# Optimization experiments

Measured on AMD Instinct MI355X. Metric: run time of the kernel, lower is better.

## Reference

```python
import jax, jax.numpy as jnp
import numpy as np

EPS = 1e-5

def _bn(x, s, b, m, v):
    # inference-mode BatchNorm2d over channel axis of NCHW
    return (x - m[None, :, None, None]) * jax.lax.rsqrt(v[None, :, None, None] + EPS) \
           * s[None, :, None, None] + b[None, :, None, None]

def _conv3(x, w):
    return jax.lax.conv_general_dilated(x, w, (1, 1), 'SAME',
                                        dimension_numbers=('NCHW', 'OIHW', 'NCHW'))

def _conv1(x, w, b):
    # 1x1 conv as einsum; w: [out_c, in_c]
    return jnp.einsum('oc,bchw->bohw', w, x) + b[None, :, None, None]

def _cca(f, qw, qb, kw, kb, vw, vb, gamma):
    # Criss-cross attention (faithful to source: no diagonal -inf masking, INF() unused there)
    B, C, H, W = f.shape
    q = _conv1(f, qw, qb)   # [B, C/8, H, W]
    k = _conv1(f, kw, kb)   # [B, C/8, H, W]
    v = _conv1(f, vw, vb)   # [B, C,   H, W]
    # energy along column (same w, all h') and row (same h, all w')
    eH = jnp.einsum('bchw,bciw->bhwi', q, k)            # [B,H,W,H]
    eW = jnp.einsum('bchw,bchj->bhwj', q, k)            # [B,H,W,W]
    att = jax.nn.softmax(jnp.concatenate([eH, eW], axis=3), axis=3)  # [B,H,W,H+W]
    aH, aW = att[..., :H], att[..., H:]
    oH = jnp.einsum('bhwi,bciw->bchw', aH, v)
    oW = jnp.einsum('bhwj,bchj->bchw', aW, v)
    return gamma * (oH + oW) + f


def setup_inputs() -> dict:
    key = jax.random.key(0)
    ks = iter(jax.random.split(key, 64))
    B, Cin, H, W = 8, 2048, 64, 64
    Ci, Cq, Co = 256, 32, 512
    rn = lambda s, sc=0.02: jax.random.normal(next(ks), s, jnp.float32) * sc
    ru = lambda s: jax.random.uniform(next(ks), s, jnp.float32)
    return {
        'x': jax.random.normal(next(ks), (B, Cin, H, W), jnp.float32),
        'recurrence': 2,
        'conva_w': rn((Ci, Cin, 3, 3)),
        'bn_a_s': ru((Ci,)), 'bn_a_b': rn((Ci,), 0.1), 'bn_a_m': rn((Ci,), 0.1), 'bn_a_v': ru((Ci,)),
        'q_w': rn((Cq, Ci)), 'q_b': rn((Cq,), 0.1),
        'k_w': rn((Cq, Ci)), 'k_b': rn((Cq,), 0.1),
        'v_w': rn((Ci, Ci)), 'v_b': rn((Ci,), 0.1),
        'cca_gamma': rn((1,), 1.0),
        'convb_w': rn((Ci, Ci, 3, 3)),
        'bn_b_s': ru((Ci,)), 'bn_b_b': rn((Ci,), 0.1), 'bn_b_m': rn((Ci,), 0.1), 'bn_b_v': ru((Ci,)),
        'sq_w': rn((Ci, Ci)), 'sq_b': rn((Ci,), 0.1),
        'bn_g_s': ru((Ci,)), 'bn_g_b': rn((Ci,), 0.1), 'bn_g_m': rn((Ci,), 0.1), 'bn_g_v': ru((Ci,)),
        'fc1_w': rn((Ci // 2, Ci)), 'fc1_b': rn((Ci // 2,), 0.1),
        'fc2_w': rn((Ci, Ci // 2)), 'fc2_b': rn((Ci,), 0.1),
        'bott_w': rn((Co, Cin + 2 * Ci, 3, 3)),
        'bn_t_s': ru((Co,)), 'bn_t_b': rn((Co,), 0.1), 'bn_t_m': rn((Co,), 0.1), 'bn_t_v': ru((Co,)),
    }


def reference(x, recurrence, conva_w, bn_a_s, bn_a_b, bn_a_m, bn_a_v,
              q_w, q_b, k_w, k_b, v_w, v_b, cca_gamma,
              convb_w, bn_b_s, bn_b_b, bn_b_m, bn_b_v,
              sq_w, sq_b, bn_g_s, bn_g_b, bn_g_m, bn_g_v,
              fc1_w, fc1_b, fc2_w, fc2_b,
              bott_w, bn_t_s, bn_t_b, bn_t_m, bn_t_v):
    out = _bn(_conv3(x, conva_w), bn_a_s, bn_a_b, bn_a_m, bn_a_v)
    # Global_Avg_Pooling (SE gating) on conva output
    fm = jax.nn.relu(_bn(_conv1(out, sq_w, sq_b), bn_g_s, bn_g_b, bn_g_m, bn_g_v))
    vec = fm.mean(axis=(-2, -1))                       # [B, Ci]
    h = jax.nn.relu(vec @ fc1_w.T + fc1_b)
    gate = jax.nn.sigmoid(h @ fc2_w.T + fc2_b)
    out_gap = out * gate[:, :, None, None]
    # recurrent criss-cross attention
    for _ in range(recurrence):
        out = _cca(out, q_w, q_b, k_w, k_b, v_w, v_b, cca_gamma)
    out = _bn(_conv3(out, convb_w), bn_b_s, bn_b_b, bn_b_m, bn_b_v)
    cat = jnp.concatenate([x, out, out_gap], axis=1)   # [B, Cin+2*Ci, H, W]
    return _bn(_conv3(cat, bott_w), bn_t_s, bn_t_b, bn_t_m, bn_t_v)
```

## Files before the change

### kernel.cpp

```cpp
#include <hip/hip_runtime.h>
#include <hip/hip_bf16.h>

typedef unsigned short u16;
typedef unsigned int u32;
typedef __attribute__((ext_vector_type(8))) short short8;
typedef __attribute__((ext_vector_type(8))) unsigned short u16x8;
typedef __attribute__((ext_vector_type(4))) float f32x4;

#define BN_EPS 1e-5f
#define PADW 66
#define CATC 2560

__device__ __forceinline__ u16 f2b(float f) {
    __hip_bfloat16 h = __float2bfloat16(f);
    return *reinterpret_cast<u16*>(&h);
}
__device__ __forceinline__ float b2f(u16 u) {
    __hip_bfloat16 h;
    *reinterpret_cast<u16*>(&h) = u;
    return __bfloat162float(h);
}
__device__ __forceinline__ void async_copy16(void* lds, const void* g) {
    __builtin_amdgcn_global_load_lds((const __attribute__((address_space(1))) u32*)g,
                                     (__attribute__((address_space(3))) u32*)lds, 16, 0, 0);
}
__device__ __forceinline__ void fence_() { asm volatile("" ::: "memory"); }
__device__ __forceinline__ void barrier_() { fence_(); __builtin_amdgcn_s_barrier(); fence_(); }

template<int TAPS, int BN, int EPI, int CPT, int NN>
__global__ __launch_bounds__(512, 2)
void gemm8(const u16* __restrict__ Ag, int cstride,
           const u16* __restrict__ Bg, int ktot,
           const float* __restrict__ alpha, const float* __restrict__ beta,
           u16* __restrict__ outb, int ostride, int ochoff,
           float* __restrict__ outf, int nch)
{
    constexpr int WN   = BN / 4;
    constexpr int NSUB = WN / 16;
    constexpr int NQ   = NSUB / 2;
    constexpr int BLH  = BN / 128;
    constexpr int ASZ  = 256 * 128;
    constexpr int BSZ  = BN * 128;
    const int KT = ktot / 64;

    extern __shared__ __align__(16) char smem[];
    char* smA = smem;
    char* smB = smem + 2 * ASZ;

    const int tid  = threadIdx.x;
    const int lane = tid & 63;
    const int wave = tid >> 6;
    const int wr = wave >> 2;
    const int wc = wave & 3;

    const int nwg = gridDim.x;
    const int wg  = blockIdx.x;
    const int swz = (wg & 7) * (nwg >> 3) + (wg >> 3);
    const int m0 = (swz / NN) * 256;
    const int n0 = (swz % NN) * BN;

    const int sr = tid >> 3;
    const int sc = tid & 7;
    const int scx8 = (sc ^ (sr & 7)) * 8;
    long apix[4];
#pragma unroll
    for (int j = 0; j < 4; ++j) {
        int p = m0 + j * 64 + sr;
        int b = p >> 12, h = (p >> 6) & 63, w = p & 63;
        apix[j] = (TAPS == 1) ? ((long)(b * PADW + h + 1) * PADW + (w + 1))
                              : ((long)(b * PADW + h) * PADW + w);
    }
    long brow[2 * BLH];
#pragma unroll
    for (int h = 0; h < 2; ++h)
#pragma unroll
        for (int l = 0; l < BLH; ++l)
            brow[h * BLH + l] = (long)(n0 + h * (BN / 2) + l * 64 + sr) * ktot;

    auto stA = [&](int bsel, int h, int c0, long toff) {
#pragma unroll
        for (int l = 0; l < 2; ++l) {
            const u16* g = Ag + (apix[2 * h + l] + toff) * cstride + c0 + scx8;
            async_copy16(smA + bsel * ASZ + h * 16384 + l * 8192 + tid * 16, g);
        }
    };
    auto stB = [&](int bsel, int h, int k0) {
#pragma unroll
        for (int l = 0; l < BLH; ++l) {
            const u16* g = Bg + brow[h * BLH + l] + k0 + scx8;
            async_copy16(smB + bsel * BSZ + h * (BSZ / 2) + l * 8192 + tid * 16, g);
        }
    };

    const int rsel  = lane & 15;
    const int cswz0 = (((lane >> 4)     ^ (lane & 7)) << 4);
    const int cswz1 = (((4 | (lane >> 4)) ^ (lane & 7)) << 4);

    f32x4 acc[8][NSUB] = {};
    short8 a[4][2], b0[NQ][2], b1[NQ][2];

    auto ldA = [&](int bsel, int mh) {
        const char* base = smA + bsel * ASZ + (wr * 128 + mh * 64 + rsel) * 128;
#pragma unroll
        for (int mi = 0; mi < 4; ++mi) {
            a[mi][0] = *(const short8*)(base + mi * 2048 + cswz0);
            a[mi][1] = *(const short8*)(base + mi * 2048 + cswz1);
        }
    };
    auto ldB = [&](int bsel, int nh, short8 (&bb)[NQ][2]) {
        const char* base = smB + bsel * BSZ + (wc * WN + nh * (WN / 2) + rsel) * 128;
#pragma unroll
        for (int nj = 0; nj < NQ; ++nj) {
            bb[nj][0] = *(const short8*)(base + nj * 2048 + cswz0);
            bb[nj][1] = *(const short8*)(base + nj * 2048 + cswz1);
        }
    };
    auto quad = [&](int MH, int NH, short8 (&bb)[NQ][2]) {
#pragma unroll
        for (int mi = 0; mi < 4; ++mi)
#pragma unroll
            for (int nj = 0; nj < NQ; ++nj)
#pragma unroll
                for (int kk = 0; kk < 2; ++kk)
                    acc[MH * 4 + mi][NH * NQ + nj] =
                        __builtin_amdgcn_mfma_f32_16x16x32_bf16(
                            a[mi][kk], bb[nj][kk], acc[MH * 4 + mi][NH * NQ + nj], 0, 0, 0);
    };

    int c0_ = 0, dx_ = 0; long toff_ = 0;
    auto adv = [&]() {
        c0_ += 64;
        if (c0_ == CPT) { c0_ = 0; toff_ += 1; if (++dx_ == 3) { dx_ = 0; toff_ += PADW - 3; } }
    };

    stA(0, 0, c0_, toff_); stA(0, 1, c0_, toff_); stB(0, 0, 0); stB(0, 1, 0);
    adv();
    stB(1, 0, 64); stB(1, 1, 64); stA(1, 0, c0_, toff_); stA(1, 1, c0_, toff_);
    int pc0 = c0_; long ptoff = toff_;
    adv();
    int skb = 128;

    if constexpr (BN == 256) asm volatile("s_waitcnt vmcnt(8)" ::: "memory");
    else                     asm volatile("s_waitcnt vmcnt(6)" ::: "memory");
    barrier_();

    for (int kt = 0; kt < KT; ++kt) {
        const int buf = kt & 1;
        ldA(buf, 0); ldB(buf, 0, b0);
        if (kt >= 1 && kt + 1 < KT) stA(buf ^ 1, 1, pc0, ptoff);
        barrier_(); asm volatile("s_waitcnt lgkmcnt(0)" ::: "memory");
        __builtin_amdgcn_s_setprio(1); quad(0, 0, b0); __builtin_amdgcn_s_setprio(0);
        barrier_();
        ldB(buf, 1, b1);
        barrier_(); asm volatile("s_waitcnt lgkmcnt(0)" ::: "memory");
        __builtin_amdgcn_s_setprio(1); quad(0, 1, b1); __builtin_amdgcn_s_setprio(0);
        barrier_();
        ldA(buf, 1);
        if (kt + 2 < KT) stB(buf, 0, skb);
        barrier_(); asm volatile("s_waitcnt lgkmcnt(0)" ::: "memory");
        __builtin_amdgcn_s_setprio(1); quad(1, 0, b0); __builtin_amdgcn_s_setprio(0);
        barrier_();
        if (kt + 2 < KT) { stB(buf, 1, skb); stA(buf, 0, c0_, toff_); }
        barrier_();
        __builtin_amdgcn_s_setprio(1); quad(1, 1, b1); __builtin_amdgcn_s_setprio(0);
        if constexpr (BN == 256) asm volatile("s_waitcnt vmcnt(6)" ::: "memory");
        else                     asm volatile("s_waitcnt vmcnt(4)" ::: "memory");
        barrier_();
        pc0 = c0_; ptoff = toff_;
        adv(); skb += 64;
    }

    const int nl = lane & 15, mq = lane >> 4;
#pragma unroll
    for (int s = 0; s < 8; ++s) {
#pragma unroll
        for (int nj = 0; nj < NSUB; ++nj) {
            int n = n0 + wc * WN + nj * 16 + nl;
            float al = alpha[n], be = beta[n];
#pragma unroll
            for (int r = 0; r < 4; ++r) {
                int m = m0 + wr * 128 + s * 16 + mq * 4 + r;
                int b = m >> 12, h = (m >> 6) & 63, w = m & 63;
                float v = acc[s][nj][r] * al + be;
                if (EPI == 0) {
                    long addr = ((long)(b * PADW + h + 1) * PADW + (w + 1)) * ostride + ochoff + n;
                    outb[addr] = f2b(v);
                } else {
                    outf[((long)(b * nch + n) << 12) + (h * 64 + w)] = v;
                }
            }
        }
    }
}

template<int TAPS, int EPI>
__global__ __launch_bounds__(256, 2)
void gemm_conv(const u16* __restrict__ A, int cstride, int cpt,
               const u16* __restrict__ Bw, int ktot,
               const float* __restrict__ alpha, const float* __restrict__ beta,
               u16* __restrict__ outb, int ostride, int ochoff,
               float* __restrict__ outf, int n_total)
{
    __shared__ u16 As[128][32];
    __shared__ u16 Bs[128][32];
    __shared__ float red[128];

    const int tid  = threadIdx.x;
    const int lane = tid & 63;
    const int wave = tid >> 6;
    const int wr = wave >> 1, wc = wave & 1;
    const int m0 = blockIdx.y * 128;
    const int n0 = blockIdx.x * 128;

    long pixbase[2];
    long browk[2];
#pragma unroll
    for (int i = 0; i < 2; ++i) {
        int row = i * 64 + (tid >> 2);
        int p = m0 + row;
        int b = p >> 12, h = (p >> 6) & 63, w = p & 63;
        if (TAPS == 1) pixbase[i] = (long)(b * PADW + h + 1) * PADW + (w + 1);
        else           pixbase[i] = (long)(b * PADW + h) * PADW + w;
        browk[i] = (long)(n0 + row) * ktot;
    }
    const int chunk = (tid & 3) * 8;

    f32x4 acc[4][4] = {};

    const int steps = ktot / 32;
    int c0 = 0, dx = 0;
    long toff = 0;
    for (int s = 0; s < steps; ++s) {
        const int k0 = s * 32;
#pragma unroll
        for (int i = 0; i < 2; ++i) {
            const u16* ga = A + (pixbase[i] + ((TAPS == 1) ? 0 : toff)) * cstride + c0 + chunk;
            async_copy16((char*)(&As[0][0]) + i * 4096 + tid * 16, ga);
            const u16* gb = Bw + browk[i] + k0 + chunk;
            async_copy16((char*)(&Bs[0][0]) + i * 4096 + tid * 16, gb);
        }
        asm volatile("s_waitcnt vmcnt(0)" ::: "memory");
        __syncthreads();

        short8 af[4], bf[4];
#pragma unroll
        for (int x = 0; x < 4; ++x) {
            af[x] = *(const short8*)&As[wr * 64 + x * 16 + (lane & 15)][(lane >> 4) * 8];
            bf[x] = *(const short8*)&Bs[wc * 64 + x * 16 + (lane & 15)][(lane >> 4) * 8];
        }
#pragma unroll
        for (int mi = 0; mi < 4; ++mi)
#pragma unroll
            for (int ni = 0; ni < 4; ++ni)
                acc[mi][ni] = __builtin_amdgcn_mfma_f32_16x16x32_bf16(af[mi], bf[ni], acc[mi][ni], 0, 0, 0);
        __syncthreads();

        c0 += 32;
        if (TAPS > 1 && c0 == cpt) {
            c0 = 0; dx++; toff += 1;
            if (dx == 3) { dx = 0; toff += PADW - 3; }
        }
    }

    const int nl = lane & 15;
    const int mq = lane >> 4;

    if (EPI == 3) {
        if (tid < 128) red[tid] = 0.f;
        __syncthreads();
#pragma unroll
        for (int ni = 0; ni < 4; ++ni) {
            int ncol = wc * 64 + ni * 16 + nl;
            int n = n0 + ncol;
            float aa = alpha[n], bb = beta[n];
            float ssum = 0.f;
#pragma unroll
            for (int mi = 0; mi < 4; ++mi)
#pragma unroll
                for (int r = 0; r < 4; ++r)
                    ssum += fmaxf(acc[mi][ni][r] * aa + bb, 0.f);
            atomicAdd(&red[ncol], ssum);
        }
        __syncthreads();
        if (tid < 128) {
            int b = m0 >> 12;
            atomicAdd(&outf[b * 256 + n0 + tid], red[tid]);
        }
    } else {
#pragma unroll
        for (int mi = 0; mi < 4; ++mi) {
#pragma unroll
            for (int r = 0; r < 4; ++r) {
                int m = m0 + wr * 64 + mi * 16 + mq * 4 + r;
                int b = m >> 12, h = (m >> 6) & 63, w = m & 63;
#pragma unroll
                for (int ni = 0; ni < 4; ++ni) {
                    int n = n0 + wc * 64 + ni * 16 + nl;
                    float v = acc[mi][ni][r] * alpha[n] + beta[n];
                    if (EPI == 0) {
                        long addr = ((long)(b * PADW + h + 1) * PADW + (w + 1)) * ostride + ochoff + n;
                        outb[addr] = f2b(v);
                    } else {
                        outb[(long)m * ostride + n] = f2b(v);
                    }
                }
            }
        }
    }
}

__global__ void xpad_k(const float* __restrict__ x, u16* __restrict__ cat)
{
    __shared__ float T[64][65];
    int bh = blockIdx.y;
    int b = bh >> 6, h = bh & 63;
    int c0 = blockIdx.x * 64;
    int t = threadIdx.x;
#pragma unroll
    for (int i = 0; i < 16; ++i) {
        int cl = i * 4 + (t >> 6);
        int w = t & 63;
        T[cl][w] = x[(((long)b * 2048 + c0 + cl) * 64 + h) * 64 + w];
    }
    __syncthreads();
#pragma unroll
    for (int i = 0; i < 16; ++i) {
        int wl = i * 4 + (t >> 6);
        int cl = t & 63;
        cat[((long)(b * PADW + h + 1) * PADW + (wl + 1)) * CATC + c0 + cl] = f2b(T[cl][wl]);
    }
}

__global__ void prep_w3(const float* __restrict__ w, u16* __restrict__ o, int O, int C)
{
    int idx = blockIdx.x * 256 + threadIdx.x;
    if (idx >= O * C) return;
    int oo = idx / C, c = idx - oo * C;
    const float* s = w + (long)idx * 9;
    long base = (long)oo * 9 * C + c;
#pragma unroll
    for (int t = 0; t < 9; ++t) o[base + (long)t * C] = f2b(s[t]);
}

__global__ void prep_qkv(const float* __restrict__ qw, const float* __restrict__ kw,
                         const float* __restrict__ vw, u16* __restrict__ o)
{
    int idx = blockIdx.x * 256 + threadIdx.x;
    int n = idx >> 8, c = idx & 255;
    float v;
    if (n < 32) v = qw[n * 256 + c];
    else if (n < 64) v = kw[(n - 32) * 256 + c];
    else if (n < 320) v = vw[(n - 64) * 256 + c];
    else v = 0.f;
    o[idx] = f2b(v);
}

__global__ void prep_cast(const float* __restrict__ w, u16* __restrict__ o, int n)
{
    int i = blockIdx.x * 256 + threadIdx.x;
    if (i < n) o[i] = f2b(w[i]);
}

__global__ void prep_ab(const float* as, const float* ab, const float* am, const float* av,
                        const float* gs, const float* gb, const float* gm, const float* gv, const float* sqb,
                        const float* bs, const float* bb, const float* bm, const float* bv,
                        const float* ts, const float* tb, const float* tm, const float* tv,
                        const float* qb, const float* kb, const float* vb,
                        float* Aa, float* Ba_, float* Ag, float* Bg, float* Ab2, float* Bb2,
                        float* At, float* Bt, float* Aq, float* Bq)
{
    int i = blockIdx.x * 256 + threadIdx.x;
    if (i < 256) { float al = as[i] * rsqrtf(av[i] + BN_EPS); Aa[i] = al; Ba_[i] = ab[i] - am[i] * al; }
    else if (i < 512) { int n = i - 256; float al = gs[n] * rsqrtf(gv[n] + BN_EPS); Ag[n] = al; Bg[n] = gb[n] - gm[n] * al + sqb[n] * al; }
    else if (i < 768) { int n = i - 512; float al = bs[n] * rsqrtf(bv[n] + BN_EPS); Ab2[n] = al; Bb2[n] = bb[n] - bm[n] * al; }
    else if (i < 1280) { int n = i - 768; float al = ts[n] * rsqrtf(tv[n] + BN_EPS); At[n] = al; Bt[n] = tb[n] - tm[n] * al; }
    else if (i < 1664) { int n = i - 1280; Aq[n] = 1.f; Bq[n] = (n < 32) ? qb[n] : (n < 64) ? kb[n - 32] : (n < 320) ? vb[n - 64] : 0.f; }
}

__global__ void gate_k(const float* __restrict__ vacc, const float* __restrict__ fc1w,
                       const float* __restrict__ fc1b, const float* __restrict__ fc2w,
                       const float* __restrict__ fc2b, float* __restrict__ gate)
{
    __shared__ float v[256], hbuf[128];
    int b = blockIdx.x, t = threadIdx.x;
    v[t] = vacc[b * 256 + t] * (1.f / 4096.f);
    __syncthreads();
    if (t < 128) {
        float s = fc1b[t];
        for (int c = 0; c < 256; ++c) s += v[c] * fc1w[t * 256 + c];
        hbuf[t] = fmaxf(s, 0.f);
    }
    __syncthreads();
    float s = fc2b[t];
    for (int j = 0; j < 128; ++j) s += hbuf[j] * fc2w[t * 128 + j];
    gate[b * 256 + t] = 1.f / (1.f + __expf(-s));
}

__global__ void gap_k(const u16* __restrict__ f0, const float* __restrict__ gate, u16* __restrict__ cat)
{
    int p = blockIdx.x, t = threadIdx.x;
    int b = p >> 12, h = (p >> 6) & 63, w = p & 63;
    long ppad = (long)(b * PADW + h + 1) * PADW + (w + 1);
    float f = b2f(f0[ppad * 256 + t]);
    cat[ppad * CATC + 2304 + t] = f2b(f * gate[b * 256 + t]);
}

__global__ void gram_k(const u16* __restrict__ qkv, float* __restrict__ e, int mode)
{
    __shared__ u16 Qs[64][32];
    __shared__ u16 Ks[64][32];
    int bx = blockIdx.x;
    int b = bx >> 6, s = bx & 63;
    int tid = threadIdx.x, lane = tid & 63, wave = tid >> 6;
    {
        int r = tid >> 2, ch = (tid & 3) * 8;
        long pix = (mode == 0) ? ((long)(b * 64 + r) * 64 + s) : ((long)(b * 64 + s) * 64 + r);
        const u16* g = qkv + pix * 384;
        *(u16x8*)&Qs[r][ch] = *(const u16x8*)(g + ch);
        *(u16x8*)&Ks[r][ch] = *(const u16x8*)(g + 32 + ch);
    }
    __syncthreads();
    f32x4 acc[4] = {};
    short8 a = *(const short8*)&Qs[wave * 16 + (lane & 15)][(lane >> 4) * 8];
#pragma unroll
    for (int ni = 0; ni < 4; ++ni) {
        short8 bb = *(const short8*)&Ks[ni * 16 + (lane & 15)][(lane >> 4) * 8];
        acc[ni] = __builtin_amdgcn_mfma_f32_16x16x32_bf16(a, bb, acc[ni], 0, 0, 0);
    }
#pragma unroll
    for (int ni = 0; ni < 4; ++ni)
#pragma unroll
        for (int r = 0; r < 4; ++r) {
            int row = wave * 16 + (lane >> 4) * 4 + r;
            int col = ni * 16 + (lane & 15);
            long pix = (mode == 0) ? ((long)(b * 64 + row) * 64 + s) : ((long)(b * 64 + s) * 64 + row);
            e[pix * 64 + col] = acc[ni][r];
        }
}

__global__ void softmax_k(const float* __restrict__ eH, const float* __restrict__ eW,
                          u16* __restrict__ aH, u16* __restrict__ aW)
{
    long row = blockIdx.x * 4 + (threadIdx.x >> 6);
    int lane = threadIdx.x & 63;
    float v0 = eH[row * 64 + lane];
    float v1 = eW[row * 64 + lane];
    float m = fmaxf(v0, v1);
#pragma unroll
    for (int off = 32; off; off >>= 1) m = fmaxf(m, __shfl_xor(m, off));
    float e0 = __expf(v0 - m), e1 = __expf(v1 - m);
    float s = e0 + e1;
#pragma unroll
    for (int off = 32; off; off >>= 1) s += __shfl_xor(s, off);
    float inv = 1.f / s;
    aH[row * 64 + lane] = f2b(e0 * inv);
    aW[row * 64 + lane] = f2b(e1 * inv);
}

__global__ __launch_bounds__(256, 2)
void oh_k(const u16* __restrict__ aH, const u16* __restrict__ qkv, float* __restrict__ oHb)
{
    __shared__ float Al[64][68];
    __shared__ u16 Vl[64][264];
    int bx = blockIdx.x;
    int b = bx >> 6, w = bx & 63;
    int t = threadIdx.x;
#pragma unroll
    for (int pass = 0; pass < 2; ++pass) {
        int r = pass * 32 + (t >> 3);
        int ch = (t & 7) * 8;
        u16x8 v = *(const u16x8*)(aH + ((long)(b * 64 + r) * 64 + w) * 64 + ch);
        f32x4 s0, s1;
#pragma unroll
        for (int u = 0; u < 4; ++u) { s0[u] = b2f(v[u]); s1[u] = b2f(v[4 + u]); }
        *(f32x4*)&Al[r][ch] = s0;
        *(f32x4*)&Al[r][ch + 4] = s1;
    }
#pragma unroll
    for (int pass = 0; pass < 8; ++pass) {
        int i = pass * 8 + (t >> 5);
        int ch = (t & 31) * 8;
        *(u16x8*)&Vl[i][ch] = *(const u16x8*)(qkv + ((long)(b * 64 + i) * 64 + w) * 384 + 64 + ch);
    }
    __syncthreads();
    int hb = (t >> 5) * 8, cb = (t & 31) * 8;
    float acc[8][8] = {};
    for (int i = 0; i < 64; ++i) {
        float av[8], vv[8];
        u16x8 v8 = *(const u16x8*)&Vl[i][cb];
#pragma unroll
        for (int u = 0; u < 8; ++u) av[u] = Al[hb + u][i];
#pragma unroll
        for (int u = 0; u < 8; ++u) vv[u] = b2f(v8[u]);
#pragma unroll
        for (int u = 0; u < 8; ++u)
#pragma unroll
            for (int x = 0; x < 8; ++x)
                acc[u][x] += av[u] * vv[x];
    }
#pragma unroll
    for (int u = 0; u < 8; ++u) {
        long base = ((long)(b * 64 + hb + u) * 64 + w) * 256 + cb;
        f32x4 s0, s1;
#pragma unroll
        for (int x = 0; x < 4; ++x) { s0[x] = acc[u][x]; s1[x] = acc[u][4 + x]; }
        *(f32x4*)&oHb[base] = s0;
        *(f32x4*)&oHb[base + 4] = s1;
    }
}

__global__ __launch_bounds__(256, 2)
void ow_k(const u16* __restrict__ aW, const u16* __restrict__ qkv, const float* __restrict__ oHb,
          const u16* __restrict__ fin, u16* __restrict__ fout, const float* __restrict__ gamma_p)
{
    __shared__ float Al[64][68];
    __shared__ u16 Vl[64][264];
    int bx = blockIdx.x;
    int b = bx >> 6, h = bx & 63;
    int t = threadIdx.x;
    float gamma = gamma_p[0];
#pragma unroll
    for (int pass = 0; pass < 2; ++pass) {
        int r = pass * 32 + (t >> 3);
        int ch = (t & 7) * 8;
        u16x8 v = *(const u16x8*)(aW + ((long)(b * 64 + h) * 64 + r) * 64 + ch);
        f32x4 s0, s1;
#pragma unroll
        for (int u = 0; u < 4; ++u) { s0[u] = b2f(v[u]); s1[u] = b2f(v[4 + u]); }
        *(f32x4*)&Al[r][ch] = s0;
        *(f32x4*)&Al[r][ch + 4] = s1;
    }
#pragma unroll
    for (int pass = 0; pass < 8; ++pass) {
        int j = pass * 8 + (t >> 5);
        int ch = (t & 31) * 8;
        *(u16x8*)&Vl[j][ch] = *(const u16x8*)(qkv + ((long)(b * 64 + h) * 64 + j) * 384 + 64 + ch);
    }
    __syncthreads();
    int wb = (t >> 5) * 8, cb = (t & 31) * 8;
    float acc[8][8] = {};
    for (int j = 0; j < 64; ++j) {
        float av[8], vv[8];
        u16x8 v8 = *(const u16x8*)&Vl[j][cb];
#pragma unroll
        for (int u = 0; u < 8; ++u) av[u] = Al[wb + u][j];
#pragma unroll
        for (int u = 0; u < 8; ++u) vv[u] = b2f(v8[u]);
#pragma unroll
        for (int u = 0; u < 8; ++u)
#pragma unroll
            for (int x = 0; x < 8; ++x)
                acc[u][x] += av[u] * vv[x];
    }
#pragma unroll
    for (int u = 0; u < 8; ++u) {
        int w = wb + u;
        long pix = ((long)(b * 64 + h) * 64 + w) * 256 + cb;
        long pp = ((long)(b * PADW + h + 1) * PADW + (w + 1)) * 256 + cb;
        u16x8 f8 = *(const u16x8*)&fin[pp];
        f32x4 o0 = *(const f32x4*)&oHb[pix];
        f32x4 o1 = *(const f32x4*)&oHb[pix + 4];
        u16x8 r8;
#pragma unroll
        for (int x = 0; x < 8; ++x) {
            float o = acc[u][x] + ((x < 4) ? o0[x] : o1[x - 4]);
            r8[x] = f2b(gamma * o + b2f(f8[x]));
        }
        *(u16x8*)&fout[pp] = r8;
    }
}

extern "C" void kernel_launch(void* const* d_in, const int* in_sizes, int n_in,
                              void* d_out, int out_size, void* d_ws, size_t ws_size,
                              hipStream_t stream)
{
    const float* x       = (const float*)d_in[0];
    const float* conva_w = (const float*)d_in[2];
    const float* bn_a_s  = (const float*)d_in[3];
    const float* bn_a_b  = (const float*)d_in[4];
    const float* bn_a_m  = (const float*)d_in[5];
    const float* bn_a_v  = (const float*)d_in[6];
    const float* q_w     = (const float*)d_in[7];
    const float* q_b     = (const float*)d_in[8];
    const float* k_w     = (const float*)d_in[9];
    const float* k_b     = (const float*)d_in[10];
    const float* v_w     = (const float*)d_in[11];
    const float* v_b     = (const float*)d_in[12];
    const float* gamma   = (const float*)d_in[13];
    const float* convb_w = (const float*)d_in[14];
    const float* bn_b_s  = (const float*)d_in[15];
    const float* bn_b_b  = (const float*)d_in[16];
    const float* bn_b_m  = (const float*)d_in[17];
    const float* bn_b_v  = (const float*)d_in[18];
    const float* sq_w    = (const float*)d_in[19];
    const float* sq_b    = (const float*)d_in[20];
    const float* bn_g_s  = (const float*)d_in[21];
    const float* bn_g_b  = (const float*)d_in[22];
    const float* bn_g_m  = (const float*)d_in[23];
    const float* bn_g_v  = (const float*)d_in[24];
    const float* fc1_w   = (const float*)d_in[25];
    const float* fc1_b   = (const float*)d_in[26];
    const float* fc2_w   = (const float*)d_in[27];
    const float* fc2_b   = (const float*)d_in[28];
    const float* bott_w  = (const float*)d_in[29];
    const float* bn_t_s  = (const float*)d_in[30];
    const float* bn_t_b  = (const float*)d_in[31];
    const float* bn_t_m  = (const float*)d_in[32];
    const float* bn_t_v  = (const float*)d_in[33];

    char* ws = (char*)d_ws;
    size_t off = 0;
    auto alloc = [&](size_t bytes) { char* p = ws + off; off += (bytes + 255) & ~(size_t)255; return p; };

    u16*   CAT  = (u16*)  alloc((size_t)8 * PADW * PADW * CATC * 2);
    u16*   F0   = (u16*)  alloc((size_t)8 * PADW * PADW * 256 * 2);
    u16*   F1   = (u16*)  alloc((size_t)8 * PADW * PADW * 256 * 2);
    u16*   QKV  = (u16*)  alloc((size_t)32768 * 384 * 2);
    float* EH   = (float*)alloc((size_t)32768 * 64 * 4);
    float* EWb  = (float*)alloc((size_t)32768 * 64 * 4);
    u16*   AH   = (u16*)  alloc((size_t)32768 * 64 * 2);
    u16*   AW   = (u16*)  alloc((size_t)32768 * 64 * 2);
    float* OHB  = (float*)alloc((size_t)32768 * 256 * 4);
    u16*   WA   = (u16*)  alloc((size_t)256 * 18432 * 2);
    u16*   WB   = (u16*)  alloc((size_t)256 * 2304 * 2);
    u16*   WT   = (u16*)  alloc((size_t)512 * 23040 * 2);
    u16*   WQKV = (u16*)  alloc((size_t)384 * 256 * 2);
    u16*   WSQ  = (u16*)  alloc((size_t)256 * 256 * 2);
    float* Aa   = (float*)alloc(256 * 4);
    float* Ba_  = (float*)alloc(256 * 4);
    float* Ag   = (float*)alloc(256 * 4);
    float* Bg   = (float*)alloc(256 * 4);
    float* Ab2  = (float*)alloc(256 * 4);
    float* Bb2  = (float*)alloc(256 * 4);
    float* At   = (float*)alloc(512 * 4);
    float* Bt   = (float*)alloc(512 * 4);
    float* Aq   = (float*)alloc(384 * 4);
    float* Bq   = (float*)alloc(384 * 4);
    float* VACC = (float*)alloc(8 * 256 * 4);
    float* GATE = (float*)alloc(8 * 256 * 4);

    hipFuncSetAttribute((const void*)gemm8<9, 128, 0, 2048, 2>,
                        hipFuncAttributeMaxDynamicSharedMemorySize, 98304);
    hipFuncSetAttribute((const void*)gemm8<9, 256, 2, 2560, 2>,
                        hipFuncAttributeMaxDynamicSharedMemorySize, 131072);

    hipMemsetAsync(CAT, 0, (size_t)8 * PADW * PADW * CATC * 2, stream);
    hipMemsetAsync(F0, 0, (size_t)2 * 8 * PADW * PADW * 256 * 2, stream);
    hipMemsetAsync(VACC, 0, 8 * 256 * 4, stream);

    prep_w3<<<(256 * 2048 + 255) / 256, 256, 0, stream>>>(conva_w, WA, 256, 2048);
    prep_w3<<<(256 * 256 + 255) / 256, 256, 0, stream>>>(convb_w, WB, 256, 256);
    prep_w3<<<(512 * 2560 + 255) / 256, 256, 0, stream>>>(bott_w, WT, 512, 2560);
    prep_qkv<<<384, 256, 0, stream>>>(q_w, k_w, v_w, WQKV);
    prep_cast<<<256, 256, 0, stream>>>(sq_w, WSQ, 65536);
    prep_ab<<<7, 256, 0, stream>>>(bn_a_s, bn_a_b, bn_a_m, bn_a_v,
                                   bn_g_s, bn_g_b, bn_g_m, bn_g_v, sq_b,
                                   bn_b_s, bn_b_b, bn_b_m, bn_b_v,
                                   bn_t_s, bn_t_b, bn_t_m, bn_t_v,
                                   q_b, k_b, v_b,
                                   Aa, Ba_, Ag, Bg, Ab2, Bb2, At, Bt, Aq, Bq);
    xpad_k<<<dim3(32, 512), 256, 0, stream>>>(x, CAT);

    gemm8<9, 128, 0, 2048, 2><<<256, 512, 98304, stream>>>(
        CAT, CATC, WA, 18432, Aa, Ba_, F0, 256, 0, nullptr, 0);
    gemm_conv<1, 3><<<dim3(2, 256), 256, 0, stream>>>(F0, 256, 256, WSQ, 256, Ag, Bg, nullptr, 0, 0, VACC, 0);
    gate_k<<<8, 256, 0, stream>>>(VACC, fc1_w, fc1_b, fc2_w, fc2_b, GATE);
    gap_k<<<32768, 256, 0, stream>>>(F0, GATE, CAT);

    for (int rec = 0; rec < 2; ++rec) {
        u16* fin = rec ? F1 : F0;
        u16* fout = rec ? F0 : F1;
        gemm_conv<1, 1><<<dim3(3, 256), 256, 0, stream>>>(fin, 256, 256, WQKV, 256, Aq, Bq, QKV, 384, 0, nullptr, 0);
        gram_k<<<512, 256, 0, stream>>>(QKV, EH, 0);
        gram_k<<<512, 256, 0, stream>>>(QKV, EWb, 1);
        softmax_k<<<8192, 256, 0, stream>>>(EH, EWb, AH, AW);
        oh_k<<<512, 256, 0, stream>>>(AH, QKV, OHB);
        ow_k<<<512, 256, 0, stream>>>(AW, QKV, OHB, fin, fout, gamma);
    }

    gemm_conv<9, 0><<<dim3(2, 256), 256, 0, stream>>>(F0, 256, 256, WB, 2304, Ab2, Bb2, CAT, CATC, 2048, nullptr, 0);
    gemm8<9, 256, 2, 2560, 2><<<256, 512, 131072, stream>>>(
        CAT, CATC, WT, 23040, At, Bt, nullptr, 0, 0, (float*)d_out, 512);
}
```

Measured before the change: 1.350 ms.

## Split-K the conva and convb 3x3 convolutions in gemm8 with a combine pass

Adds a KSPLIT parameter to gemm8 so the conva and convb convolutions run as full-width (BN=256) tiles with K split in two. Each half writes fp32 partials into a workspace aliased over the CCA buffers, and a new combine_k kernel sums them, applies BN and writes bf16 into the padded destination. Convb moves from the small gemm_conv kernel to the pipelined gemm8 path. This keeps the 256-block grid while loading each A tile once for all 256 output channels, at the cost of extra fp32 partial traffic and an extra launch. The final-iteration wait is also tightened to vmcnt(0) for correctness with shorter K loops.

```diff
diff --git a/kernel.cpp b/kernel.cpp
--- a/kernel.cpp
+++ b/kernel.cpp
@@ -27,10 +27,10 @@
 __device__ __forceinline__ void fence_() { asm volatile("" ::: "memory"); }
 __device__ __forceinline__ void barrier_() { fence_(); __builtin_amdgcn_s_barrier(); fence_(); }
 
-template<int TAPS, int BN, int EPI, int CPT, int NN>
+template<int TAPS, int BN, int EPI, int CPT, int NTILES, int KSPLIT>
 __global__ __launch_bounds__(512, 2)
 void gemm8(const u16* __restrict__ Ag, int cstride,
-           const u16* __restrict__ Bg, int ktot,
+           const u16* __restrict__ Bg, int ktot_full, int klen,
            const float* __restrict__ alpha, const float* __restrict__ beta,
            u16* __restrict__ outb, int ostride, int ochoff,
            float* __restrict__ outf, int nch)
@@ -41,7 +41,7 @@
     constexpr int BLH  = BN / 128;
     constexpr int ASZ  = 256 * 128;
     constexpr int BSZ  = BN * 128;
-    const int KT = ktot / 64;
+    const int KT = klen / 64;
 
     extern __shared__ __align__(16) char smem[];
     char* smA = smem;
@@ -56,8 +56,11 @@
     const int nwg = gridDim.x;
     const int wg  = blockIdx.x;
     const int swz = (wg & 7) * (nwg >> 3) + (wg >> 3);
-    const int m0 = (swz / NN) * 256;
-    const int n0 = (swz % NN) * BN;
+    const int sel = swz % (NTILES * KSPLIT);
+    const int m0  = (swz / (NTILES * KSPLIT)) * 256;
+    const int n0  = (sel / KSPLIT) * BN;
+    const int ks  = sel % KSPLIT;
+    const int kstart = ks * klen;
 
     const int sr = tid >> 3;
     const int sc = tid & 7;
@@ -75,7 +78,7 @@
     for (int h = 0; h < 2; ++h)
 #pragma unroll
         for (int l = 0; l < BLH; ++l)
-            brow[h * BLH + l] = (long)(n0 + h * (BN / 2) + l * 64 + sr) * ktot;
+            brow[h * BLH + l] = (long)(n0 + h * (BN / 2) + l * 64 + sr) * ktot_full;
 
     auto stA = [&](int bsel, int h, int c0, long toff) {
 #pragma unroll
@@ -127,18 +130,21 @@
                             a[mi][kk], bb[nj][kk], acc[MH * 4 + mi][NH * NQ + nj], 0, 0, 0);
     };
 
-    int c0_ = 0, dx_ = 0; long toff_ = 0;
+    const int tap0 = kstart / CPT;
+    int c0_ = kstart - tap0 * CPT;
+    int dx_ = tap0 % 3;
+    long toff_ = dx_ + (long)(tap0 / 3) * PADW;
     auto adv = [&]() {
         c0_ += 64;
         if (c0_ == CPT) { c0_ = 0; toff_ += 1; if (++dx_ == 3) { dx_ = 0; toff_ += PADW - 3; } }
     };
 
-    stA(0, 0, c0_, toff_); stA(0, 1, c0_, toff_); stB(0, 0, 0); stB(0, 1, 0);
+    stA(0, 0, c0_, toff_); stA(0, 1, c0_, toff_); stB(0, 0, kstart); stB(0, 1, kstart);
     adv();
-    stB(1, 0, 64); stB(1, 1, 64); stA(1, 0, c0_, toff_); stA(1, 1, c0_, toff_);
+    stB(1, 0, kstart + 64); stB(1, 1, kstart + 64); stA(1, 0, c0_, toff_); stA(1, 1, c0_, toff_);
     int pc0 = c0_; long ptoff = toff_;
     adv();
-    int skb = 128;
+    int skb = kstart + 128;
 
     if constexpr (BN == 256) asm volatile("s_waitcnt vmcnt(8)" ::: "memory");
     else                     asm volatile("s_waitcnt vmcnt(6)" ::: "memory");
@@ -163,8 +169,13 @@
         if (kt + 2 < KT) { stB(buf, 1, skb); stA(buf, 0, c0_, toff_); }
         barrier_();
         __builtin_amdgcn_s_setprio(1); quad(1, 1, b1); __builtin_amdgcn_s_setprio(0);
-        if constexpr (BN == 256) asm volatile("s_waitcnt vmcnt(6)" ::: "memory");
-        else                     asm volatile("s_waitcnt vmcnt(4)" ::: "memory");
+        if (kt + 2 >= KT) {
+            asm volatile("s_waitcnt vmcnt(0)" ::: "memory");
+        } else if constexpr (BN == 256) {
+            asm volatile("s_waitcnt vmcnt(6)" ::: "memory");
+        } else {
+            asm volatile("s_waitcnt vmcnt(4)" ::: "memory");
+        }
         barrier_();
         pc0 = c0_; ptoff = toff_;
         adv(); skb += 64;
@@ -176,21 +187,36 @@
 #pragma unroll
         for (int nj = 0; nj < NSUB; ++nj) {
             int n = n0 + wc * WN + nj * 16 + nl;
-            float al = alpha[n], be = beta[n];
+            float al = (EPI == 4) ? 1.f : alpha[n];
+            float be = (EPI == 4) ? 0.f : beta[n];
 #pragma unroll
             for (int r = 0; r < 4; ++r) {
                 int m = m0 + wr * 128 + s * 16 + mq * 4 + r;
-                int b = m >> 12, h = (m >> 6) & 63, w = m & 63;
                 float v = acc[s][nj][r] * al + be;
                 if (EPI == 0) {
+                    int b = m >> 12, h = (m >> 6) & 63, w = m & 63;
                     long addr = ((long)(b * PADW + h + 1) * PADW + (w + 1)) * ostride + ochoff + n;
                     outb[addr] = f2b(v);
+                } else if (EPI == 2) {
+                    int b = m >> 12, h = (m >> 6) & 63, w = m & 63;
+                    outf[((long)(b * nch + n) << 12) + (h * 64 + w)] = v;
                 } else {
-                    outf[((long)(b * nch + n) << 12) + (h * 64 + w)] = v;
+                    outf[(long)ks * ((long)32768 * nch) + (long)m * nch + n] = v;
                 }
             }
         }
     }
+}
+
+__global__ void combine_k(const float* __restrict__ P,
+                          const float* __restrict__ alpha, const float* __restrict__ beta,
+                          u16* __restrict__ dst, int dstride, int choff)
+{
+    int m = blockIdx.x, n = threadIdx.x;
+    int b = m >> 12, h = (m >> 6) & 63, w = m & 63;
+    float v = P[(long)m * 256 + n] + P[(long)32768 * 256 + (long)m * 256 + n];
+    v = v * alpha[n] + beta[n];
+    dst[((long)(b * PADW + h + 1) * PADW + (w + 1)) * dstride + choff + n] = f2b(v);
 }
 
 template<int TAPS, int EPI>
@@ -292,17 +318,11 @@
 #pragma unroll
             for (int r = 0; r < 4; ++r) {
                 int m = m0 + wr * 64 + mi * 16 + mq * 4 + r;
-                int b = m >> 12, h = (m >> 6) & 63, w = m & 63;
 #pragma unroll
                 for (int ni = 0; ni < 4; ++ni) {
                     int n = n0 + wc * 64 + ni * 16 + nl;
                     float v = acc[mi][ni][r] * alpha[n] + beta[n];
-                    if (EPI == 0) {
-                        long addr = ((long)(b * PADW + h + 1) * PADW + (w + 1)) * ostride + ochoff + n;
-                        outb[addr] = f2b(v);
-                    } else {
-                        outb[(long)m * ostride + n] = f2b(v);
-                    }
+                    outb[(long)m * ostride + n] = f2b(v);
                 }
             }
         }
@@ -615,12 +635,14 @@
     u16*   CAT  = (u16*)  alloc((size_t)8 * PADW * PADW * CATC * 2);
     u16*   F0   = (u16*)  alloc((size_t)8 * PADW * PADW * 256 * 2);
     u16*   F1   = (u16*)  alloc((size_t)8 * PADW * PADW * 256 * 2);
+    size_t cca_off = off;
     u16*   QKV  = (u16*)  alloc((size_t)32768 * 384 * 2);
     float* EH   = (float*)alloc((size_t)32768 * 64 * 4);
     float* EWb  = (float*)alloc((size_t)32768 * 64 * 4);
     u16*   AH   = (u16*)  alloc((size_t)32768 * 64 * 2);
     u16*   AW   = (u16*)  alloc((size_t)32768 * 64 * 2);
     float* OHB  = (float*)alloc((size_t)32768 * 256 * 4);
+    float* P    = (float*)(ws + cca_off);
     u16*   WA   = (u16*)  alloc((size_t)256 * 18432 * 2);
     u16*   WB   = (u16*)  alloc((size_t)256 * 2304 * 2);
     u16*   WT   = (u16*)  alloc((size_t)512 * 23040 * 2);
@@ -639,9 +661,11 @@
     float* VACC = (float*)alloc(8 * 256 * 4);
     float* GATE = (float*)alloc(8 * 256 * 4);
 
-    hipFuncSetAttribute((const void*)gemm8<9, 128, 0, 2048, 2>,
-                        hipFuncAttributeMaxDynamicSharedMemorySize, 98304);
-    hipFuncSetAttribute((const void*)gemm8<9, 256, 2, 2560, 2>,
+    hipFuncSetAttribute((const void*)gemm8<9, 256, 4, 2048, 1, 2>,
+                        hipFuncAttributeMaxDynamicSharedMemorySize, 131072);
+    hipFuncSetAttribute((const void*)gemm8<9, 256, 4, 256, 1, 2>,
+                        hipFuncAttributeMaxDynamicSharedMemorySize, 131072);
+    hipFuncSetAttribute((const void*)gemm8<9, 256, 2, 2560, 2, 1>,
                         hipFuncAttributeMaxDynamicSharedMemorySize, 131072);
 
     hipMemsetAsync(CAT, 0, (size_t)8 * PADW * PADW * CATC * 2, stream);
@@ -661,8 +685,10 @@
                                    Aa, Ba_, Ag, Bg, Ab2, Bb2, At, Bt, Aq, Bq);
     xpad_k<<<dim3(32, 512), 256, 0, stream>>>(x, CAT);
 
-    gemm8<9, 128, 0, 2048, 2><<<256, 512, 98304, stream>>>(
-        CAT, CATC, WA, 18432, Aa, Ba_, F0, 256, 0, nullptr, 0);
+    gemm8<9, 256, 4, 2048, 1, 2><<<256, 512, 131072, stream>>>(
+        CAT, CATC, WA, 18432, 9216, Aa, Ba_, nullptr, 0, 0, P, 256);
+    combine_k<<<32768, 256, 0, stream>>>(P, Aa, Ba_, F0, 256, 0);
+
     gemm_conv<1, 3><<<dim3(2, 256), 256, 0, stream>>>(F0, 256, 256, WSQ, 256, Ag, Bg, nullptr, 0, 0, VACC, 0);
     gate_k<<<8, 256, 0, stream>>>(VACC, fc1_w, fc1_b, fc2_w, fc2_b, GATE);
     gap_k<<<32768, 256, 0, stream>>>(F0, GATE, CAT);
@@ -678,7 +704,10 @@
         ow_k<<<512, 256, 0, stream>>>(AW, QKV, OHB, fin, fout, gamma);
     }
 
-    gemm_conv<9, 0><<<dim3(2, 256), 256, 0, stream>>>(F0, 256, 256, WB, 2304, Ab2, Bb2, CAT, CATC, 2048, nullptr, 0);
-    gemm8<9, 256, 2, 2560, 2><<<256, 512, 131072, stream>>>(
-        CAT, CATC, WT, 23040, At, Bt, nullptr, 0, 0, (float*)d_out, 512);
-}
+    gemm8<9, 256, 4, 256, 1, 2><<<256, 512, 131072, stream>>>(
+        F0, 256, WB, 2304, 1152, Ab2, Bb2, nullptr, 0, 0, P, 256);
+    combine_k<<<32768, 256, 0, stream>>>(P, Ab2, Bb2, CAT, CATC, 2048);
+
+    gemm8<9, 256, 2, 2560, 2, 1><<<256, 512, 131072, stream>>>(
+        CAT, CATC, WT, 23040, 23040, At, Bt, nullptr, 0, 0, (float*)d_out, 512);
+}
```

New measurement: 1.315 ms. -2.6%, faster.
